# Optimization experiments

Measured on AMD Instinct MI355X. Metric: run time of the kernel, lower is better.

Reference implementation:

```python
import jax, jax.numpy as jnp
import numpy as np

B, T, C = 2, 2048, 1024
H = 16
D = C // H  # head_dim = 64


def setup_inputs() -> dict:
    key = jax.random.key(0)
    ks = jax.random.split(key, 9)
    s = 0.02
    return {
        "x": jax.random.normal(ks[0], (B, T, C), dtype=jnp.float32),
        "Wq": jax.random.normal(ks[1], (C, C), dtype=jnp.float32) * s,
        "bq": jax.random.normal(ks[2], (C,), dtype=jnp.float32) * s,
        "Wk": jax.random.normal(ks[3], (C, C), dtype=jnp.float32) * s,
        "bk": jax.random.normal(ks[4], (C,), dtype=jnp.float32) * s,
        "Wv": jax.random.normal(ks[5], (C, C), dtype=jnp.float32) * s,
        "bv": jax.random.normal(ks[6], (C,), dtype=jnp.float32) * s,
        "Wo": jax.random.normal(ks[7], (C, C), dtype=jnp.float32) * s,
        "bo": jax.random.normal(ks[8], (C,), dtype=jnp.float32) * s,
    }


def reference(x, Wq, bq, Wk, bk, Wv, bv, Wo, bo):
    b, t, c = x.shape
    h, d = H, c // H
    # torch nn.Linear: y = x @ W.T + b
    q = (x @ Wq.T + bq).reshape(b, t, h, d).transpose(0, 2, 1, 3)  # [B,H,T,D]
    k = (x @ Wk.T + bk).reshape(b, t, h, d).transpose(0, 2, 1, 3)
    v = (x @ Wv.T + bv).reshape(b, t, h, d).transpose(0, 2, 1, 3)

    scores = jnp.einsum("bhqd,bhkd->bhqk", q, k) / jnp.sqrt(jnp.float32(d))
    causal = jnp.tril(jnp.ones((t, t), dtype=bool))  # [T,T]
    scores = jnp.where(causal[None, None, :, :], scores, -jnp.inf)
    attn = jax.nn.softmax(scores, axis=-1)  # [B,H,T,T]

    out = jnp.einsum("bhqk,bhkd->bhqd", attn, v)  # [B,H,T,D]
    out = out.transpose(0, 2, 1, 3).reshape(b, t, c)
    out = out @ Wo.T + bo
    return out
```

## Files before the change

### kernel.cpp

```cpp
#include <hip/hip_runtime.h>
#include <hip/hip_bf16.h>

using u16 = unsigned short;
using u32 = unsigned int;
using short8  = __attribute__((ext_vector_type(8))) short;
using short4v = __attribute__((ext_vector_type(4))) short;
using floatx4 = __attribute__((ext_vector_type(4))) float;

#define TT 2048
#define CC 1024
#define HH 16
#define DD 64
#define BBATCH 2
#define MM (BBATCH*TT)

#define QSCALE 0.18033688011112042f

__device__ __forceinline__ u16 f2bf(float f) {
    u32 u = __float_as_uint(f);
    u += 0x7fffu + ((u >> 16) & 1u);
    return (u16)(u >> 16);
}
__device__ __forceinline__ float bf2f(u16 s) {
    return __uint_as_float(((u32)s) << 16);
}
__device__ __forceinline__ float bpermf(float v, int srclane) {
    return __int_as_float(__builtin_amdgcn_ds_bpermute(srclane * 4, __float_as_int(v)));
}
__device__ __forceinline__ void gll16(const u16* g, u16* l) {
    __builtin_amdgcn_global_load_lds((const __attribute__((address_space(1))) void*)g,
                                     (__attribute__((address_space(3))) void*)l, 16, 0, 0);
}

__global__ __launch_bounds__(256) void cast_all(const float* __restrict__ x,
    const float* __restrict__ Wq, const float* __restrict__ Wk,
    const float* __restrict__ Wv, const float* __restrict__ Wo,
    u16* __restrict__ xb, u16* __restrict__ wqb, u16* __restrict__ wkb,
    u16* __restrict__ wvb, u16* __restrict__ wob)
{
    int i = blockIdx.x * 256 + threadIdx.x;
    const float* src; u16* dst; int off;
    if (i < 1048576) { src = x; dst = xb; off = i; }
    else {
        int j = i - 1048576;
        int s = j >> 18;
        off = j & 262143;
        src = (s == 0) ? Wq : (s == 1) ? Wk : (s == 2) ? Wv : Wo;
        dst = (s == 0) ? wqb : (s == 1) ? wkb : (s == 2) ? wvb : wob;
    }
    float4 v = ((const float4*)src)[off];
    u16 r[4];
    r[0] = f2bf(v.x); r[1] = f2bf(v.y); r[2] = f2bf(v.z); r[3] = f2bf(v.w);
    ((ushort4*)dst)[off] = *(ushort4*)r;
}

__global__ __launch_bounds__(256) void transpose_v(const u16* __restrict__ v, u16* __restrict__ vt) {
    __shared__ u16 tile[64][72];
    int bh = blockIdx.y;
    int t0 = blockIdx.x * 64;
    int r = threadIdx.x >> 2;
    int c = (threadIdx.x & 3) * 16;
    const u16* src = v + ((size_t)bh * TT + t0 + r) * DD + c;
    *(uint4*)&tile[r][c]     = *(const uint4*)src;
    *(uint4*)&tile[r][c + 8] = *(const uint4*)(src + 8);
    __syncthreads();
    u16 tmp[16];
#pragma unroll
    for (int j = 0; j < 16; ++j) tmp[j] = tile[c + j][r];
    u16* dst = vt + ((size_t)bh * DD + r) * TT + t0 + c;
    *(uint4*)dst       = *(uint4*)&tmp[0];
    *(uint4*)(dst + 8) = *(uint4*)&tmp[8];
}

__global__ __launch_bounds__(256, 2) void qkv_gemm(const u16* __restrict__ xb,
    const u16* __restrict__ wq, const u16* __restrict__ wk, const u16* __restrict__ wv,
    const float* __restrict__ bq, const float* __restrict__ bk, const float* __restrict__ bv,
    u16* __restrict__ q, u16* __restrict__ k, u16* __restrict__ v)
{
    __shared__ u16 As[128*32];
    __shared__ u16 Bs[128*32];
    const int K = CC;
    int z = blockIdx.z;
    const u16* W = (z == 0) ? wq : (z == 1) ? wk : wv;
    const float* bias = (z == 0) ? bq : (z == 1) ? bk : bv;
    u16* outp = (z == 0) ? q : (z == 1) ? k : v;
    float outscale = (z == 0) ? QSCALE : 1.0f;

    int tid = threadIdx.x;
    int m0 = blockIdx.y * 128;
    int n0 = blockIdx.x * 128;
    int lane = tid & 63;
    int w  = tid >> 6;
    int wm = (w >> 1) * 64;
    int wn = (w & 1) * 64;
    int lm = lane & 15;
    int lq = lane >> 4;

    floatx4 acc[4][4];
#pragma unroll
    for (int i = 0; i < 4; ++i)
#pragma unroll
        for (int j = 0; j < 4; ++j)
            acc[i][j] = (floatx4){0.f, 0.f, 0.f, 0.f};

    const u16* ag = xb + (size_t)(m0 + (tid >> 2)) * K + (tid & 3) * 8;
    const u16* wg = W  + (size_t)(n0 + (tid >> 2)) * K + (tid & 3) * 8;
    u16* asl = As + tid * 8;
    u16* bsl = Bs + tid * 8;

    for (int k0 = 0; k0 < K; k0 += 32) {
        __syncthreads();
        gll16(ag + k0,           asl);
        gll16(ag + 64*K + k0,    asl + 2048);
        gll16(wg + k0,           bsl);
        gll16(wg + 64*K + k0,    bsl + 2048);
        __syncthreads();
        short8 af[4], bfr[4];
#pragma unroll
        for (int t = 0; t < 4; ++t) {
            af[t]  = *(const short8*)(As + (wm + t*16 + lm)*32 + lq*8);
            bfr[t] = *(const short8*)(Bs + (wn + t*16 + lm)*32 + lq*8);
        }
#pragma unroll
        for (int i = 0; i < 4; ++i)
#pragma unroll
            for (int j = 0; j < 4; ++j)
                acc[i][j] = __builtin_amdgcn_mfma_f32_16x16x32_bf16(af[i], bfr[j], acc[i][j], 0, 0, 0);
    }

#pragma unroll
    for (int j = 0; j < 4; ++j) {
        int col = n0 + wn + j*16 + lm;
        float bv2 = bias[col];
#pragma unroll
        for (int i = 0; i < 4; ++i) {
#pragma unroll
            for (int r = 0; r < 4; ++r) {
                int row = m0 + wm + i*16 + lq*4 + r;
                float val = (acc[i][j][r] + bv2) * outscale;
                int b_ = row >> 11, t_ = row & (TT-1);
                int h_ = col >> 6,  d_ = col & 63;
                outp[(((size_t)(b_*HH + h_) * TT + t_) * DD) + d_] = f2bf(val);
            }
        }
    }
}

__global__ __launch_bounds__(256, 4) void o_gemm(const u16* __restrict__ A, const u16* __restrict__ W,
                                                 const float* __restrict__ bias, float* __restrict__ outp)
{
    __shared__ u16 As[128*32];
    __shared__ u16 Bs[64*32];
    const int K = CC;
    int tid = threadIdx.x;
    int m0 = blockIdx.y * 128;
    int n0 = blockIdx.x * 64;
    int lane = tid & 63;
    int w  = tid >> 6;
    int lm = lane & 15;
    int lq = lane >> 4;

    floatx4 acc[2][4];
#pragma unroll
    for (int i = 0; i < 2; ++i)
#pragma unroll
        for (int j = 0; j < 4; ++j)
            acc[i][j] = (floatx4){0.f, 0.f, 0.f, 0.f};

    const u16* ag = A + (size_t)(m0 + (tid >> 2)) * K + (tid & 3) * 8;
    const u16* wg = W + (size_t)(n0 + (tid >> 2)) * K + (tid & 3) * 8;
    u16* asl = As + tid * 8;
    u16* bsl = Bs + tid * 8;

    for (int k0 = 0; k0 < K; k0 += 32) {
        __syncthreads();
        gll16(ag + k0,        asl);
        gll16(ag + 64*K + k0, asl + 2048);
        gll16(wg + k0,        bsl);
        __syncthreads();
        short8 af[2], bfr[4];
#pragma unroll
        for (int i = 0; i < 2; ++i)
            af[i] = *(const short8*)(As + (w*32 + i*16 + lm)*32 + lq*8);
#pragma unroll
        for (int j = 0; j < 4; ++j)
            bfr[j] = *(const short8*)(Bs + (j*16 + lm)*32 + lq*8);
#pragma unroll
        for (int i = 0; i < 2; ++i)
#pragma unroll
            for (int j = 0; j < 4; ++j)
                acc[i][j] = __builtin_amdgcn_mfma_f32_16x16x32_bf16(af[i], bfr[j], acc[i][j], 0, 0, 0);
    }

#pragma unroll
    for (int j = 0; j < 4; ++j) {
        int col = n0 + j*16 + lm;
        float bv2 = bias[col];
#pragma unroll
        for (int i = 0; i < 2; ++i) {
#pragma unroll
            for (int r = 0; r < 4; ++r) {
                int row = m0 + w*32 + i*16 + lq*4 + r;
                outp[(size_t)row * CC + col] = acc[i][j][r] + bv2;
            }
        }
    }
}

__global__ __launch_bounds__(128, 2) void attn_mfma(const u16* __restrict__ qg, const u16* __restrict__ kg,
                                                    const u16* __restrict__ vtg, u16* __restrict__ attnb)
{
    __shared__ u16 Ks[64*64];
    __shared__ u16 Vs[64*72];

    int tid = threadIdx.x;
    int lane = tid & 63;
    int w = tid >> 6;
    int lm = lane & 15;
    int lq = lane >> 4;
    int qt = 31 - (int)blockIdx.x;
    int bh = blockIdx.y;
    int b_ = bh >> 4, h_ = bh & 15;
    int q0 = qt * 64;

    const size_t basek  = (size_t)bh * TT * DD;
    const size_t basevt = (size_t)bh * DD * TT;

    short8 aq[2][2];
    {
        const u16* qbase = qg + basek + (size_t)(q0 + w*32 + lm) * DD + lq*8;
#pragma unroll
        for (int i = 0; i < 2; ++i)
#pragma unroll
            for (int ks = 0; ks < 2; ++ks)
                aq[i][ks] = *(const short8*)(qbase + i*16*DD + ks*32);
    }

    floatx4 oacc[2][4];
#pragma unroll
    for (int i = 0; i < 2; ++i)
#pragma unroll
        for (int j = 0; j < 4; ++j)
            oacc[i][j] = (floatx4){0.f, 0.f, 0.f, 0.f};
    float mrun[2] = {-3e38f, -3e38f};
    float lrun[2] = {0.f, 0.f};

    const u16* kgl = kg + basek + (size_t)(w*32 + (lane >> 3)) * DD + (lane & 7) * 8;
    u16* kls = Ks + w*32*64 + lane*8;
    int vrow = tid >> 1;
    int kbv  = (tid & 1) * 2;
    const u16* vsrc = vtg + basevt + (size_t)vrow * TT + kbv*16;
    u16* vdst0 = Vs + vrow*72 + (kbv>>1)*32 + (kbv&1)*4;
    u16* vdst1 = Vs + vrow*72 + ((kbv+1)>>1)*32 + ((kbv+1)&1)*4;

    int nkt = qt + 1;

    for (int kt = 0; kt < nkt; ++kt) {
        uint4 v0a = *(const uint4*)(vsrc + kt*64);
        uint4 v0b = *(const uint4*)(vsrc + kt*64 + 8);
        uint4 v1a = *(const uint4*)(vsrc + kt*64 + 16);
        uint4 v1b = *(const uint4*)(vsrc + kt*64 + 24);
        __syncthreads();
#pragma unroll
        for (int c = 0; c < 4; ++c)
            gll16(kgl + (size_t)(kt*64 + c*8) * DD, kls + c*512);
        *(uint2*)(vdst0)      = make_uint2(v0a.x, v0a.y);
        *(uint2*)(vdst0 + 8)  = make_uint2(v0a.z, v0a.w);
        *(uint2*)(vdst0 + 16) = make_uint2(v0b.x, v0b.y);
        *(uint2*)(vdst0 + 24) = make_uint2(v0b.z, v0b.w);
        *(uint2*)(vdst1)      = make_uint2(v1a.x, v1a.y);
        *(uint2*)(vdst1 + 8)  = make_uint2(v1a.z, v1a.w);
        *(uint2*)(vdst1 + 16) = make_uint2(v1b.x, v1b.y);
        *(uint2*)(vdst1 + 24) = make_uint2(v1b.z, v1b.w);
        __syncthreads();

        floatx4 st[2][4];
#pragma unroll
        for (int i = 0; i < 2; ++i)
#pragma unroll
            for (int jn = 0; jn < 4; ++jn)
                st[i][jn] = (floatx4){0.f, 0.f, 0.f, 0.f};
#pragma unroll
        for (int jn = 0; jn < 4; ++jn) {
            short8 kf0 = *(const short8*)&Ks[(jn*16 + lm)*64 + lq*8];
            short8 kf1 = *(const short8*)&Ks[(jn*16 + lm)*64 + 32 + lq*8];
#pragma unroll
            for (int i = 0; i < 2; ++i) {
                st[i][jn] = __builtin_amdgcn_mfma_f32_16x16x32_bf16(kf0, aq[i][0], st[i][jn], 0, 0, 0);
                st[i][jn] = __builtin_amdgcn_mfma_f32_16x16x32_bf16(kf1, aq[i][1], st[i][jn], 0, 0, 0);
            }
        }

        int kbase = kt*64;
        short4v ap[2][4];
#pragma unroll
        for (int i = 0; i < 2; ++i) {
            int qrow = q0 + w*32 + i*16 + lm;
            if (kbase + 63 > q0 + w*32 + i*16) {
#pragma unroll
                for (int jn = 0; jn < 4; ++jn)
#pragma unroll
                    for (int r = 0; r < 4; ++r) {
                        int key = kbase + jn*16 + lq*4 + r;
                        if (key > qrow) st[i][jn][r] = -__builtin_inff();
                    }
            }
            float mx = st[i][0][0];
#pragma unroll
            for (int jn = 0; jn < 4; ++jn)
#pragma unroll
                for (int r = 0; r < 4; ++r) mx = fmaxf(mx, st[i][jn][r]);
            mx = fmaxf(mx, __shfl_xor(mx, 16));
            mx = fmaxf(mx, __shfl_xor(mx, 32));
            float mold = mrun[i];
            float newm = fmaxf(mold, mx);
            mrun[i] = newm;
            float psum = 0.f;
#pragma unroll
            for (int jn = 0; jn < 4; ++jn)
#pragma unroll
                for (int r = 0; r < 4; ++r) {
                    float pe = __builtin_amdgcn_exp2f(st[i][jn][r] - newm);
                    st[i][jn][r] = pe;
                    psum += pe;
                }
            psum += __shfl_xor(psum, 16);
            psum += __shfl_xor(psum, 32);
            float alpha = __builtin_amdgcn_exp2f(mold - newm);
            lrun[i] = lrun[i]*alpha + psum;
#pragma unroll
            for (int jn = 0; jn < 4; ++jn) {
                u32 lo = __builtin_amdgcn_perm(__float_as_uint(st[i][jn][1]),
                                               __float_as_uint(st[i][jn][0]), 0x07060302u);
                u32 hi = __builtin_amdgcn_perm(__float_as_uint(st[i][jn][3]),
                                               __float_as_uint(st[i][jn][2]), 0x07060302u);
                uint2 pk = make_uint2(lo, hi);
                ap[i][jn] = __builtin_bit_cast(short4v, pk);
            }
            if (__ballot(newm != mold)) {
                float ar[4];
#pragma unroll
                for (int r = 0; r < 4; ++r) ar[r] = bpermf(alpha, lq*4 + r);
#pragma unroll
                for (int jd = 0; jd < 4; ++jd)
#pragma unroll
                    for (int r = 0; r < 4; ++r) oacc[i][jd][r] *= ar[r];
            }
        }

#pragma unroll
        for (int p2 = 0; p2 < 2; ++p2) {
#pragma unroll
            for (int jd = 0; jd < 4; ++jd) {
                short8 vb = *(const short8*)&Vs[(jd*16 + lm)*72 + p2*32 + lq*8];
                short4v blo, bhi;
#pragma unroll
                for (int j = 0; j < 4; ++j) { blo[j] = vb[j]; bhi[j] = vb[j+4]; }
#pragma unroll
                for (int i = 0; i < 2; ++i) {
                    oacc[i][jd] = __builtin_amdgcn_mfma_f32_16x16x16bf16_1k(ap[i][2*p2],   blo, oacc[i][jd], 0, 0, 0);
                    oacc[i][jd] = __builtin_amdgcn_mfma_f32_16x16x16bf16_1k(ap[i][2*p2+1], bhi, oacc[i][jd], 0, 0, 0);
                }
            }
        }
    }

#pragma unroll
    for (int i = 0; i < 2; ++i) {
        float il[4];
#pragma unroll
        for (int r = 0; r < 4; ++r) il[r] = 1.f / bpermf(lrun[i], lq*4 + r);
#pragma unroll
        for (int r = 0; r < 4; ++r) {
            int qrow = q0 + w*32 + i*16 + lq*4 + r;
            u16* orow = attnb + ((size_t)(b_*TT + qrow)) * CC + h_*DD + lm;
#pragma unroll
            for (int jd = 0; jd < 4; ++jd)
                orow[jd*16] = f2bf(oacc[i][jd][r] * il[r]);
        }
    }
}

extern "C" void kernel_launch(void* const* d_in, const int* in_sizes, int n_in,
                              void* d_out, int out_size, void* d_ws, size_t ws_size,
                              hipStream_t stream)
{
    const float* x  = (const float*)d_in[0];
    const float* Wq = (const float*)d_in[1];
    const float* bq = (const float*)d_in[2];
    const float* Wk = (const float*)d_in[3];
    const float* bk = (const float*)d_in[4];
    const float* Wv = (const float*)d_in[5];
    const float* bv = (const float*)d_in[6];
    const float* Wo = (const float*)d_in[7];
    const float* bo = (const float*)d_in[8];
    float* out = (float*)d_out;

    char* ws = (char*)d_ws;
    u16* xb   = (u16*)(ws);
    u16* wqb  = (u16*)(ws + (size_t)( 8<<20));
    u16* wkb  = (u16*)(ws + (size_t)(10<<20));
    u16* wvb  = (u16*)(ws + (size_t)(12<<20));
    u16* wob  = (u16*)(ws + (size_t)(14<<20));
    u16* q    = (u16*)(ws + (size_t)(16<<20));
    u16* k    = (u16*)(ws + (size_t)(24<<20));
    u16* v    = (u16*)(ws + (size_t)(32<<20));
    u16* vt   = (u16*)(ws + (size_t)(40<<20));
    u16* attnb = xb;

    cast_all<<<dim3(8192), dim3(256), 0, stream>>>(x, Wq, Wk, Wv, Wo, xb, wqb, wkb, wvb, wob);

    dim3 gq(CC/128, MM/128, 3);
    qkv_gemm<<<gq, dim3(256), 0, stream>>>(xb, wqb, wkb, wvb, bq, bk, bv, q, k, v);

    transpose_v<<<dim3(TT/64, BBATCH*HH), dim3(256), 0, stream>>>(v, vt);

    attn_mfma<<<dim3(TT/64, BBATCH*HH), dim3(128), 0, stream>>>(q, k, vt, attnb);

    dim3 go(CC/64, MM/128);
    o_gemm<<<go, dim3(256), 0, stream>>>(attnb, wob, bo, out);
}
```

Baseline: 219.9 us.

## Fuse V transpose into QKV epilogue and drop LDS staging in attention

The QKV GEMM epilogue now writes V directly in transposed [B,H,D,T] layout, which removes the separate transpose_v kernel and its extra round trip through memory. The attention kernel no longer stages K and V tiles in shared memory with barriers. Each wave loads its K and V fragments straight from global memory into registers and works independently on a 32-row query strip. The four waves of a 256-thread block take mirrored strips so causal work is balanced across waves and blocks. The cost is redundant global and L2 reads of K and V by every wave, plus higher register pressure.

```diff
diff --git a/kernel.cpp b/kernel.cpp
--- a/kernel.cpp
+++ b/kernel.cpp
@@ -20,9 +20,6 @@
     u32 u = __float_as_uint(f);
     u += 0x7fffu + ((u >> 16) & 1u);
     return (u16)(u >> 16);
-}
-__device__ __forceinline__ float bf2f(u16 s) {
-    return __uint_as_float(((u32)s) << 16);
 }
 __device__ __forceinline__ float bpermf(float v, int srclane) {
     return __int_as_float(__builtin_amdgcn_ds_bpermute(srclane * 4, __float_as_int(v)));
@@ -54,28 +51,10 @@
     ((ushort4*)dst)[off] = *(ushort4*)r;
 }
 
-__global__ __launch_bounds__(256) void transpose_v(const u16* __restrict__ v, u16* __restrict__ vt) {
-    __shared__ u16 tile[64][72];
-    int bh = blockIdx.y;
-    int t0 = blockIdx.x * 64;
-    int r = threadIdx.x >> 2;
-    int c = (threadIdx.x & 3) * 16;
-    const u16* src = v + ((size_t)bh * TT + t0 + r) * DD + c;
-    *(uint4*)&tile[r][c]     = *(const uint4*)src;
-    *(uint4*)&tile[r][c + 8] = *(const uint4*)(src + 8);
-    __syncthreads();
-    u16 tmp[16];
-#pragma unroll
-    for (int j = 0; j < 16; ++j) tmp[j] = tile[c + j][r];
-    u16* dst = vt + ((size_t)bh * DD + r) * TT + t0 + c;
-    *(uint4*)dst       = *(uint4*)&tmp[0];
-    *(uint4*)(dst + 8) = *(uint4*)&tmp[8];
-}
-
 __global__ __launch_bounds__(256, 2) void qkv_gemm(const u16* __restrict__ xb,
     const u16* __restrict__ wq, const u16* __restrict__ wk, const u16* __restrict__ wv,
     const float* __restrict__ bq, const float* __restrict__ bk, const float* __restrict__ bv,
-    u16* __restrict__ q, u16* __restrict__ k, u16* __restrict__ v)
+    u16* __restrict__ q, u16* __restrict__ k, u16* __restrict__ vt)
 {
     __shared__ u16 As[128*32];
     __shared__ u16 Bs[128*32];
@@ -83,7 +62,6 @@
     int z = blockIdx.z;
     const u16* W = (z == 0) ? wq : (z == 1) ? wk : wv;
     const float* bias = (z == 0) ? bq : (z == 1) ? bk : bv;
-    u16* outp = (z == 0) ? q : (z == 1) ? k : v;
     float outscale = (z == 0) ? QSCALE : 1.0f;
 
     int tid = threadIdx.x;
@@ -128,19 +106,38 @@
                 acc[i][j] = __builtin_amdgcn_mfma_f32_16x16x32_bf16(af[i], bfr[j], acc[i][j], 0, 0, 0);
     }
 
-#pragma unroll
-    for (int j = 0; j < 4; ++j) {
-        int col = n0 + wn + j*16 + lm;
-        float bv2 = bias[col];
-#pragma unroll
-        for (int i = 0; i < 4; ++i) {
-#pragma unroll
-            for (int r = 0; r < 4; ++r) {
-                int row = m0 + wm + i*16 + lq*4 + r;
-                float val = (acc[i][j][r] + bv2) * outscale;
-                int b_ = row >> 11, t_ = row & (TT-1);
-                int h_ = col >> 6,  d_ = col & 63;
-                outp[(((size_t)(b_*HH + h_) * TT + t_) * DD) + d_] = f2bf(val);
+    if (z < 2) {
+        u16* outp = (z == 0) ? q : k;
+#pragma unroll
+        for (int j = 0; j < 4; ++j) {
+            int col = n0 + wn + j*16 + lm;
+            float bv2 = bias[col];
+            int h_ = col >> 6, d_ = col & 63;
+#pragma unroll
+            for (int i = 0; i < 4; ++i) {
+#pragma unroll
+                for (int r = 0; r < 4; ++r) {
+                    int row = m0 + wm + i*16 + lq*4 + r;
+                    float val = (acc[i][j][r] + bv2) * outscale;
+                    int b_ = row >> 11, t_ = row & (TT-1);
+                    outp[(((size_t)(b_*HH + h_) * TT + t_) * DD) + d_] = f2bf(val);
+                }
+            }
+        }
+    } else {
+#pragma unroll
+        for (int j = 0; j < 4; ++j) {
+            int col = n0 + wn + j*16 + lm;
+            float bv2 = bias[col];
+            int h_ = col >> 6, d_ = col & 63;
+#pragma unroll
+            for (int i = 0; i < 4; ++i) {
+                int row0 = m0 + wm + i*16 + lq*4;
+                int b_ = row0 >> 11, t_ = row0 & (TT-1);
+                u16 rr[4];
+#pragma unroll
+                for (int r = 0; r < 4; ++r) rr[r] = f2bf(acc[i][j][r] + bv2);
+                *(ushort4*)(vt + ((size_t)(b_*HH + h_) * DD + d_) * TT + t_) = *(ushort4*)rr;
             }
         }
     }
@@ -207,28 +204,26 @@
     }
 }
 
-__global__ __launch_bounds__(128, 2) void attn_mfma(const u16* __restrict__ qg, const u16* __restrict__ kg,
+__global__ __launch_bounds__(256, 2) void attn_mfma(const u16* __restrict__ qg, const u16* __restrict__ kg,
                                                     const u16* __restrict__ vtg, u16* __restrict__ attnb)
 {
-    __shared__ u16 Ks[64*64];
-    __shared__ u16 Vs[64*72];
-
     int tid = threadIdx.x;
     int lane = tid & 63;
     int w = tid >> 6;
     int lm = lane & 15;
     int lq = lane >> 4;
-    int qt = 31 - (int)blockIdx.x;
-    int bh = blockIdx.y;
+    int blk = blockIdx.x;
+    int bh  = blockIdx.y;
     int b_ = bh >> 4, h_ = bh & 15;
-    int q0 = qt * 64;
+    int s = (w == 0) ? blk : (w == 1) ? (31 - blk) : (w == 2) ? (32 + blk) : (63 - blk);
+    int q0 = s * 32;
 
     const size_t basek  = (size_t)bh * TT * DD;
     const size_t basevt = (size_t)bh * DD * TT;
 
     short8 aq[2][2];
     {
-        const u16* qbase = qg + basek + (size_t)(q0 + w*32 + lm) * DD + lq*8;
+        const u16* qbase = qg + basek + (size_t)(q0 + lm) * DD + lq*8;
 #pragma unroll
         for (int i = 0; i < 2; ++i)
 #pragma unroll
@@ -245,34 +240,27 @@
     float mrun[2] = {-3e38f, -3e38f};
     float lrun[2] = {0.f, 0.f};
 
-    const u16* kgl = kg + basek + (size_t)(w*32 + (lane >> 3)) * DD + (lane & 7) * 8;
-    u16* kls = Ks + w*32*64 + lane*8;
-    int vrow = tid >> 1;
-    int kbv  = (tid & 1) * 2;
-    const u16* vsrc = vtg + basevt + (size_t)vrow * TT + kbv*16;
-    u16* vdst0 = Vs + vrow*72 + (kbv>>1)*32 + (kbv&1)*4;
-    u16* vdst1 = Vs + vrow*72 + ((kbv+1)>>1)*32 + ((kbv+1)&1)*4;
-
-    int nkt = qt + 1;
+    const u16* kfp = kg  + basek  + (size_t)lm * DD + lq*8;
+    const u16* vfp = vtg + basevt + (size_t)lm * TT + lq*4;
+
+    int nkt = (s >> 1) + 1;
 
     for (int kt = 0; kt < nkt; ++kt) {
-        uint4 v0a = *(const uint4*)(vsrc + kt*64);
-        uint4 v0b = *(const uint4*)(vsrc + kt*64 + 8);
-        uint4 v1a = *(const uint4*)(vsrc + kt*64 + 16);
-        uint4 v1b = *(const uint4*)(vsrc + kt*64 + 24);
-        __syncthreads();
-#pragma unroll
-        for (int c = 0; c < 4; ++c)
-            gll16(kgl + (size_t)(kt*64 + c*8) * DD, kls + c*512);
-        *(uint2*)(vdst0)      = make_uint2(v0a.x, v0a.y);
-        *(uint2*)(vdst0 + 8)  = make_uint2(v0a.z, v0a.w);
-        *(uint2*)(vdst0 + 16) = make_uint2(v0b.x, v0b.y);
-        *(uint2*)(vdst0 + 24) = make_uint2(v0b.z, v0b.w);
-        *(uint2*)(vdst1)      = make_uint2(v1a.x, v1a.y);
-        *(uint2*)(vdst1 + 8)  = make_uint2(v1a.z, v1a.w);
-        *(uint2*)(vdst1 + 16) = make_uint2(v1b.x, v1b.y);
-        *(uint2*)(vdst1 + 24) = make_uint2(v1b.z, v1b.w);
-        __syncthreads();
+        int kbase = kt * 64;
+        short8 kf[4][2];
+#pragma unroll
+        for (int jn = 0; jn < 4; ++jn)
+#pragma unroll
+            for (int ks = 0; ks < 2; ++ks)
+                kf[jn][ks] = *(const short8*)(kfp + (size_t)(kbase + jn*16) * DD + ks*32);
+        short4v vf[4][4];
+#pragma unroll
+        for (int jd = 0; jd < 4; ++jd)
+#pragma unroll
+            for (int kb = 0; kb < 4; ++kb) {
+                uint2 raw = *(const uint2*)(vfp + (size_t)(jd*16) * TT + kbase + kb*16);
+                vf[jd][kb] = __builtin_bit_cast(short4v, raw);
+            }
 
         floatx4 st[2][4];
 #pragma unroll
@@ -281,22 +269,18 @@
             for (int jn = 0; jn < 4; ++jn)
                 st[i][jn] = (floatx4){0.f, 0.f, 0.f, 0.f};
 #pragma unroll
-        for (int jn = 0; jn < 4; ++jn) {
-            short8 kf0 = *(const short8*)&Ks[(jn*16 + lm)*64 + lq*8];
-            short8 kf1 = *(const short8*)&Ks[(jn*16 + lm)*64 + 32 + lq*8];
+        for (int jn = 0; jn < 4; ++jn)
 #pragma unroll
             for (int i = 0; i < 2; ++i) {
-                st[i][jn] = __builtin_amdgcn_mfma_f32_16x16x32_bf16(kf0, aq[i][0], st[i][jn], 0, 0, 0);
-                st[i][jn] = __builtin_amdgcn_mfma_f32_16x16x32_bf16(kf1, aq[i][1], st[i][jn], 0, 0, 0);
-            }
-        }
-
-        int kbase = kt*64;
+                st[i][jn] = __builtin_amdgcn_mfma_f32_16x16x32_bf16(kf[jn][0], aq[i][0], st[i][jn], 0, 0, 0);
+                st[i][jn] = __builtin_amdgcn_mfma_f32_16x16x32_bf16(kf[jn][1], aq[i][1], st[i][jn], 0, 0, 0);
+            }
+
         short4v ap[2][4];
 #pragma unroll
         for (int i = 0; i < 2; ++i) {
-            int qrow = q0 + w*32 + i*16 + lm;
-            if (kbase + 63 > q0 + w*32 + i*16) {
+            int qrow = q0 + i*16 + lm;
+            if (kbase + 63 > q0 + i*16) {
 #pragma unroll
                 for (int jn = 0; jn < 4; ++jn)
 #pragma unroll
@@ -349,20 +333,12 @@
         }
 
 #pragma unroll
-        for (int p2 = 0; p2 < 2; ++p2) {
-#pragma unroll
-            for (int jd = 0; jd < 4; ++jd) {
-                short8 vb = *(const short8*)&Vs[(jd*16 + lm)*72 + p2*32 + lq*8];
-                short4v blo, bhi;
-#pragma unroll
-                for (int j = 0; j < 4; ++j) { blo[j] = vb[j]; bhi[j] = vb[j+4]; }
-#pragma unroll
-                for (int i = 0; i < 2; ++i) {
-                    oacc[i][jd] = __builtin_amdgcn_mfma_f32_16x16x16bf16_1k(ap[i][2*p2],   blo, oacc[i][jd], 0, 0, 0);
-                    oacc[i][jd] = __builtin_amdgcn_mfma_f32_16x16x16bf16_1k(ap[i][2*p2+1], bhi, oacc[i][jd], 0, 0, 0);
-                }
-            }
-        }
+        for (int kb = 0; kb < 4; ++kb)
+#pragma unroll
+            for (int jd = 0; jd < 4; ++jd)
+#pragma unroll
+                for (int i = 0; i < 2; ++i)
+                    oacc[i][jd] = __builtin_amdgcn_mfma_f32_16x16x16bf16_1k(ap[i][kb], vf[jd][kb], oacc[i][jd], 0, 0, 0);
     }
 
 #pragma unroll
@@ -372,7 +348,7 @@
         for (int r = 0; r < 4; ++r) il[r] = 1.f / bpermf(lrun[i], lq*4 + r);
 #pragma unroll
         for (int r = 0; r < 4; ++r) {
-            int qrow = q0 + w*32 + i*16 + lq*4 + r;
+            int qrow = q0 + i*16 + lq*4 + r;
             u16* orow = attnb + ((size_t)(b_*TT + qrow)) * CC + h_*DD + lm;
 #pragma unroll
             for (int jd = 0; jd < 4; ++jd)
@@ -404,18 +380,15 @@
     u16* wob  = (u16*)(ws + (size_t)(14<<20));
     u16* q    = (u16*)(ws + (size_t)(16<<20));
     u16* k    = (u16*)(ws + (size_t)(24<<20));
-    u16* v    = (u16*)(ws + (size_t)(32<<20));
-    u16* vt   = (u16*)(ws + (size_t)(40<<20));
+    u16* vt   = (u16*)(ws + (size_t)(32<<20));
     u16* attnb = xb;
 
     cast_all<<<dim3(8192), dim3(256), 0, stream>>>(x, Wq, Wk, Wv, Wo, xb, wqb, wkb, wvb, wob);
 
     dim3 gq(CC/128, MM/128, 3);
-    qkv_gemm<<<gq, dim3(256), 0, stream>>>(xb, wqb, wkb, wvb, bq, bk, bv, q, k, v);
-
-    transpose_v<<<dim3(TT/64, BBATCH*HH), dim3(256), 0, stream>>>(v, vt);
-
-    attn_mfma<<<dim3(TT/64, BBATCH*HH), dim3(128), 0, stream>>>(q, k, vt, attnb);
+    qkv_gemm<<<gq, dim3(256), 0, stream>>>(xb, wqb, wkb, wvb, bq, bk, bv, q, k, vt);
+
+    attn_mfma<<<dim3(16, BBATCH*HH), dim3(256), 0, stream>>>(q, k, vt, attnb);
 
     dim3 go(CC/64, MM/128);
     o_gemm<<<go, dim3(256), 0, stream>>>(attnb, wob, bo, out);
```

Measured after the change: 241.3 us. +9.7%, slower.
